# Optimization experiments

Hardware: AMD Instinct MI355X
Metric: run time of the kernel (lower is better)

## Reference

```python
import jax, jax.numpy as jnp
import numpy as np

N = 30000        # nodes
E = 480000       # edges
IN_DIM = 128
HID = 64
OUT = 64
POS_DIM = 32
H = 4            # heads (same for all layers)
PVOCAB = 3
NEG_SLOPE = 0.2


def _xavier(key, shape):
    fan_in, fan_out = shape[0], shape[-1] if len(shape) > 1 else shape[0]
    scale = 1.414 * np.sqrt(2.0 / (fan_in + fan_out))
    return jax.random.normal(key, shape, dtype=jnp.float32) * scale


def setup_inputs() -> dict:
    key = jax.random.key(0)
    ks = jax.random.split(key, 20)
    d0_in = IN_DIM + POS_DIM            # 160
    d_mid = HID * H + POS_DIM           # 288
    inp = {
        "features": jax.random.normal(ks[0], (N, IN_DIM), dtype=jnp.float32),
        # layer 0
        "W0": _xavier(ks[1], (d0_in, H * HID)),
        "al0": _xavier(ks[2], (H, HID)),
        "ar0": _xavier(ks[3], (H, HID)),
        "pe0": _xavier(ks[4], (PVOCAB, POS_DIM)),
        # layer 1
        "W1": _xavier(ks[5], (d_mid, H * HID)),
        "al1": _xavier(ks[6], (H, HID)),
        "ar1": _xavier(ks[7], (H, HID)),
        "pe1": _xavier(ks[8], (PVOCAB, POS_DIM)),
        # output layer
        "W2": _xavier(ks[9], (d_mid, H * OUT)),
        "al2": _xavier(ks[10], (H, OUT)),
        "ar2": _xavier(ks[11], (H, OUT)),
        "pe2": _xavier(ks[12], (PVOCAB, POS_DIM)),
        # graph
        "src": jax.random.randint(ks[13], (E,), 0, N, dtype=jnp.int32),
        "dst": jax.random.randint(ks[14], (E,), 0, N, dtype=jnp.int32),
        "pos": jax.random.randint(ks[15], (N,), 0, PVOCAB, dtype=jnp.int32),
    }
    return inp


def gat_layer(h, W, a_l, a_r, src, dst):
    # h: [N, in_d]; W: [in_d, H*d]; a_l,a_r: [H, d]
    n = h.shape[0]
    nh, d = a_l.shape
    ft = (h @ W).reshape(n, nh, d)                       # [N,H,d]
    a1 = jnp.einsum("nhd,hd->nh", ft, a_l)               # [N,H]
    a2 = jnp.einsum("nhd,hd->nh", ft, a_r)               # [N,H]
    e = jax.nn.leaky_relu(a1[src] + a2[dst], NEG_SLOPE)  # [E,H]
    # per-destination segment softmax (numerically stable)
    m = jax.ops.segment_max(e, dst, num_segments=n)      # [N,H]
    ex = jnp.exp(e - m[dst])                             # [E,H]
    s = jax.ops.segment_sum(ex, dst, num_segments=n)     # [N,H]
    alpha = ex / s[dst]                                  # [E,H]
    msg = ft[src] * alpha[:, :, None]                    # [E,H,d]
    return jax.ops.segment_sum(msg, dst, num_segments=n) # [N,H,d]


def reference(features, W0, al0, ar0, pe0, W1, al1, ar1, pe1,
              W2, al2, ar2, pe2, src, dst, pos):
    h = features
    # hidden GAT layers with ELU activation and head-flattening
    for W, al, ar, pe in ((W0, al0, ar0, pe0), (W1, al1, ar1, pe1)):
        p = pe[pos]                                      # [N, pos_dim]
        hcat = jnp.concatenate((h, p), axis=1)
        out = gat_layer(hcat, W, al, ar, src, dst)       # [N,H,d]
        h = jax.nn.elu(out.reshape(out.shape[0], -1))    # [N,H*d]
    # output layer: mean over heads
    p = pe2[pos]
    hcat = jnp.concatenate((h, p), axis=1)
    out = gat_layer(hcat, W2, al2, ar2, src, dst)        # [N,H,out]
    return out.mean(axis=1)                              # [N,out]
```

## Files before the change

kernel.cpp:

```cpp
#include <hip/hip_runtime.h>
#include <hip/hip_fp16.h>
#include <math.h>

#define N_NODES 30000
#define N_EDGES 480000
#define HEADS 4
#define DHEAD 64
#define FDIM 256
#define POSD 32
#define SCAN_B 1024
#define SCAN_NB ((N_NODES + SCAN_B - 1) / SCAN_B)

typedef _Float16 half8 __attribute__((ext_vector_type(8)));
typedef float floatx4 __attribute__((ext_vector_type(4)));

__device__ __forceinline__ float lrelu(float x){ return x > 0.f ? x : 0.2f * x; }

__global__ void hist_k(const int* __restrict__ dst, int* __restrict__ deg){
  int e = blockIdx.x * blockDim.x + threadIdx.x;
  if (e < N_EDGES) atomicAdd(&deg[dst[e]], 1);
}

__global__ void scanA_k(const int* __restrict__ deg, int* __restrict__ off,
                        int* __restrict__ bsum){
  __shared__ int sm[SCAN_B];
  int t = threadIdx.x;
  int i = blockIdx.x * SCAN_B + t;
  int x = (i < N_NODES) ? deg[i] : 0;
  sm[t] = x;
  __syncthreads();
#pragma unroll
  for (int o = 1; o < SCAN_B; o <<= 1){
    int v = (t >= o) ? sm[t - o] : 0;
    __syncthreads();
    sm[t] += v;
    __syncthreads();
  }
  if (i < N_NODES) off[i] = sm[t] - x;
  if (t == SCAN_B - 1) bsum[blockIdx.x] = sm[t];
}

__global__ void scanB_k(int* __restrict__ bsum, int* __restrict__ boff){
  __shared__ int sm[64];
  int t = threadIdx.x;
  int x = (t < SCAN_NB) ? bsum[t] : 0;
  sm[t] = x;
  __syncthreads();
#pragma unroll
  for (int o = 1; o < 64; o <<= 1){
    int v = (t >= o) ? sm[t - o] : 0;
    __syncthreads();
    sm[t] += v;
    __syncthreads();
  }
  if (t < SCAN_NB) boff[t] = sm[t] - x;
}

__global__ void scanC_k(int* __restrict__ off, const int* __restrict__ boff,
                        int* __restrict__ cursor){
  int i = blockIdx.x * SCAN_B + threadIdx.x;
  if (i < N_NODES){
    int v = off[i] + boff[blockIdx.x];
    off[i] = v;
    cursor[i] = v;
  }
  if (i == 0) off[N_NODES] = N_EDGES;
}

__global__ void scatter_k(const int* __restrict__ src, const int* __restrict__ dst,
                          int* __restrict__ cursor, int* __restrict__ esrc){
  int e = blockIdx.x * blockDim.x + threadIdx.x;
  if (e < N_EDGES){
    int d = dst[e];
    int p = atomicAdd(&cursor[d], 1);
    esrc[p] = src[e];
  }
}

__global__ __launch_bounds__(256) void prep_k(
    const float* __restrict__ features, _Float16* __restrict__ feat16,
    const float* __restrict__ W0, const float* __restrict__ W1,
    const float* __restrict__ W2, _Float16* __restrict__ T0,
    _Float16* __restrict__ T1, _Float16* __restrict__ T2,
    const float* __restrict__ pe0, const float* __restrict__ pe1,
    const float* __restrict__ pe2, float* __restrict__ PW){
  int blk = blockIdx.x;
  if (blk < 3750){
    int i = (blk * 256 + threadIdx.x) * 4;
    float4 v = *(const float4*)&features[i];
    struct h4s { _Float16 h[4]; } u;
    u.h[0] = (_Float16)v.x; u.h[1] = (_Float16)v.y;
    u.h[2] = (_Float16)v.z; u.h[3] = (_Float16)v.w;
    *(h4s*)&feat16[i] = u;
  } else if (blk < 3942){
    int q = blk - 3750;
    int l = q >> 6, kk0 = q & 63;
    const float* W = l == 0 ? W0 : (l == 1 ? W1 : W2);
    _Float16* T    = l == 0 ? T0 : (l == 1 ? T1 : T2);
    int K = l == 0 ? 128 : 256;
    int n = threadIdx.x;
    for (int k = kk0; k < K; k += 64)
      T[(size_t)n * K + k] = (_Float16)W[(size_t)k * FDIM + n];
  } else {
    int q = blk - 3942;
    int layer = q / 3, v = q % 3;
    const float* W  = layer == 0 ? W0 : (layer == 1 ? W1 : W2);
    const float* pe = layer == 0 ? pe0 : (layer == 1 ? pe1 : pe2);
    int K = layer == 0 ? 128 : 256;
    int j = threadIdx.x;
    float s = 0.f;
#pragma unroll
    for (int k = 0; k < POSD; k++)
      s = fmaf(pe[v * POSD + k], W[(size_t)(K + k) * FDIM + j], s);
    PW[(layer * 3 + v) * FDIM + j] = s;
  }
}

__global__ __launch_bounds__(256) void gemm_mfma_k(
    const _Float16* __restrict__ A, const _Float16* __restrict__ Wt,
    const float* __restrict__ PW, const int* __restrict__ pos,
    const float* __restrict__ al, const float* __restrict__ arw,
    _Float16* __restrict__ Ch, float* __restrict__ a1, float* __restrict__ a2,
    int K){
  int t = threadIdx.x;
  int w = t >> 6;
  int lane = t & 63;
  int lm = lane & 15;
  int kq = lane >> 4;
  int h = blockIdx.x;
  int rowBase = blockIdx.y * 256 + w * 64;
  int colBase = h * 64;

  floatx4 acc[4][4] = {};

  const _Float16* Ar[4];
#pragma unroll
  for (int r = 0; r < 4; r++)
    Ar[r] = A + (size_t)min(rowBase + r * 16 + lm, N_NODES - 1) * K;
  const _Float16* B0 = Wt + (size_t)(colBase + 0 * 16 + lm) * K;
  const _Float16* B1 = Wt + (size_t)(colBase + 1 * 16 + lm) * K;
  const _Float16* B2 = Wt + (size_t)(colBase + 2 * 16 + lm) * K;
  const _Float16* B3 = Wt + (size_t)(colBase + 3 * 16 + lm) * K;

  for (int kb = 0; kb < K; kb += 32){
    int ko = kb + kq * 8;
    half8 b0 = *(const half8*)(B0 + ko);
    half8 b1 = *(const half8*)(B1 + ko);
    half8 b2 = *(const half8*)(B2 + ko);
    half8 b3 = *(const half8*)(B3 + ko);
#pragma unroll
    for (int r = 0; r < 4; r++){
      half8 af = *(const half8*)(Ar[r] + ko);
      acc[r][0] = __builtin_amdgcn_mfma_f32_16x16x32_f16(af, b0, acc[r][0], 0, 0, 0);
      acc[r][1] = __builtin_amdgcn_mfma_f32_16x16x32_f16(af, b1, acc[r][1], 0, 0, 0);
      acc[r][2] = __builtin_amdgcn_mfma_f32_16x16x32_f16(af, b2, acc[r][2], 0, 0, 0);
      acc[r][3] = __builtin_amdgcn_mfma_f32_16x16x32_f16(af, b3, acc[r][3], 0, 0, 0);
    }
  }

  float alw[4], arr[4];
#pragma unroll
  for (int j = 0; j < 4; j++){
    alw[j] = al [h * DHEAD + j * 16 + lm];
    arr[j] = arw[h * DHEAD + j * 16 + lm];
  }

#pragma unroll
  for (int r = 0; r < 4; r++){
#pragma unroll
    for (int p = 0; p < 4; p++){
      int row = rowBase + r * 16 + kq * 4 + p;
      if (row >= N_NODES) continue;
      int pz = pos[row];
      const float* pwb = PW + pz * FDIM + colBase;
      float s1 = 0.f, s2 = 0.f;
#pragma unroll
      for (int j = 0; j < 4; j++){
        float v = acc[r][j][p] + pwb[j * 16 + lm];
        Ch[(size_t)row * FDIM + colBase + j * 16 + lm] = (_Float16)v;
        s1 = fmaf(v, alw[j], s1);
        s2 = fmaf(v, arr[j], s2);
      }
      s1 += __shfl_xor(s1, 1, 64); s2 += __shfl_xor(s2, 1, 64);
      s1 += __shfl_xor(s1, 2, 64); s2 += __shfl_xor(s2, 2, 64);
      s1 += __shfl_xor(s1, 4, 64); s2 += __shfl_xor(s2, 4, 64);
      s1 += __shfl_xor(s1, 8, 64); s2 += __shfl_xor(s2, 8, 64);
      if (lm == 0){
        a1[row * HEADS + h] = s1;
        a2[row * HEADS + h] = s2;
      }
    }
  }
}

__global__ __launch_bounds__(256) void agg4_k(
    const _Float16* __restrict__ ft, const float* __restrict__ a1,
    const float* __restrict__ a2, const int* __restrict__ off,
    const int* __restrict__ esrc, _Float16* __restrict__ outh,
    float* __restrict__ outf, int mode){
  int wv = threadIdx.x >> 6;
  int lane = threadIdx.x & 63;
  int n = blockIdx.x * 4 + wv;
  if (n >= N_NODES) return;
  int jb = off[n];
  int deg = off[n + 1] - jb;
  int eidx = lane & 15, h = lane >> 4;
  int hsel = h << 4;
  float a2n = a2[n * HEADS + h];
  float4 acc = make_float4(0.f, 0.f, 0.f, 0.f);
  const _Float16* ftl = ft + lane * 4;

  if (deg <= 64){
    int sreg[4]; float wreg[4];
    float m = -INFINITY;
#pragma unroll
    for (int r = 0; r < 4; r++){
      int idx = eidx + r * 16;
      int s = (idx < deg) ? esrc[jb + idx] : 0;
      sreg[r] = s;
      float e = (idx < deg) ? lrelu(a1[s * HEADS + h] + a2n) : -INFINITY;
      wreg[r] = e;
      m = fmaxf(m, e);
    }
    m = fmaxf(m, __shfl_xor(m, 1, 64));
    m = fmaxf(m, __shfl_xor(m, 2, 64));
    m = fmaxf(m, __shfl_xor(m, 4, 64));
    m = fmaxf(m, __shfl_xor(m, 8, 64));
    float ss = 0.f;
#pragma unroll
    for (int r = 0; r < 4; r++){
      int idx = eidx + r * 16;
      float tv = (idx < deg) ? __expf(wreg[r] - m) : 0.f;
      wreg[r] = tv;
      ss += tv;
    }
    ss += __shfl_xor(ss, 1, 64);
    ss += __shfl_xor(ss, 2, 64);
    ss += __shfl_xor(ss, 4, 64);
    ss += __shfl_xor(ss, 8, 64);
    float inv = (ss > 0.f) ? 1.f / ss : 0.f;
#pragma unroll
    for (int r = 0; r < 4; r++) wreg[r] *= inv;

#pragma unroll
    for (int r = 0; r < 4; r++){
      if (r * 16 >= deg) break;
      int lim = deg - r * 16; if (lim > 16) lim = 16;
      float wr = wreg[r]; int sr = sreg[r];
      for (int jj = 0; jj < lim; jj += 4){
#pragma unroll
        for (int u = 0; u < 4; u++){
          float wj = __shfl(wr, (jj + u) | hsel, 64);
          int sj = __shfl(sr, jj + u, 64);
          struct h4 { __half2 a, b; };
          h4 f = *(const h4*)(ftl + (size_t)sj * FDIM);
          float2 fa = __half22float2(f.a), fb = __half22float2(f.b);
          acc.x = fmaf(wj, fa.x, acc.x);
          acc.y = fmaf(wj, fa.y, acc.y);
          acc.z = fmaf(wj, fb.x, acc.z);
          acc.w = fmaf(wj, fb.y, acc.w);
        }
      }
    }
  } else {
    float m = -INFINITY;
    for (int idx = eidx; idx < deg; idx += 16){
      int s = esrc[jb + idx];
      m = fmaxf(m, lrelu(a1[s * HEADS + h] + a2n));
    }
    m = fmaxf(m, __shfl_xor(m, 1, 64));
    m = fmaxf(m, __shfl_xor(m, 2, 64));
    m = fmaxf(m, __shfl_xor(m, 4, 64));
    m = fmaxf(m, __shfl_xor(m, 8, 64));
    float ss = 0.f;
    for (int idx = eidx; idx < deg; idx += 16){
      int s = esrc[jb + idx];
      ss += __expf(lrelu(a1[s * HEADS + h] + a2n) - m);
    }
    ss += __shfl_xor(ss, 1, 64);
    ss += __shfl_xor(ss, 2, 64);
    ss += __shfl_xor(ss, 4, 64);
    ss += __shfl_xor(ss, 8, 64);
    float inv = (ss > 0.f) ? 1.f / ss : 0.f;
    for (int j = 0; j < deg; j++){
      int sj = esrc[jb + j];
      float e = lrelu(a1[sj * HEADS + h] + a2n);
      float wj = __expf(e - m) * inv;
      struct h4 { __half2 a, b; };
      h4 f = *(const h4*)(ftl + (size_t)sj * FDIM);
      float2 fa = __half22float2(f.a), fb = __half22float2(f.b);
      acc.x = fmaf(wj, fa.x, acc.x);
      acc.y = fmaf(wj, fa.y, acc.y);
      acc.z = fmaf(wj, fb.x, acc.z);
      acc.w = fmaf(wj, fb.y, acc.w);
    }
  }

  if (mode == 0){
    acc.x = acc.x > 0.f ? acc.x : (__expf(acc.x) - 1.f);
    acc.y = acc.y > 0.f ? acc.y : (__expf(acc.y) - 1.f);
    acc.z = acc.z > 0.f ? acc.z : (__expf(acc.z) - 1.f);
    acc.w = acc.w > 0.f ? acc.w : (__expf(acc.w) - 1.f);
    struct h4s { _Float16 h[4]; } u;
    u.h[0] = (_Float16)acc.x; u.h[1] = (_Float16)acc.y;
    u.h[2] = (_Float16)acc.z; u.h[3] = (_Float16)acc.w;
    *(h4s*)&outh[(size_t)n * FDIM + lane * 4] = u;
  } else {
#pragma unroll
    for (int o2 = 16; o2 <= 32; o2 <<= 1){
      acc.x += __shfl_xor(acc.x, o2, 64);
      acc.y += __shfl_xor(acc.y, o2, 64);
      acc.z += __shfl_xor(acc.z, o2, 64);
      acc.w += __shfl_xor(acc.w, o2, 64);
    }
    if (lane < 16){
      float4 o;
      o.x = acc.x * 0.25f; o.y = acc.y * 0.25f;
      o.z = acc.z * 0.25f; o.w = acc.w * 0.25f;
      *(float4*)&outf[(size_t)n * DHEAD + lane * 4] = o;
    }
  }
}

extern "C" void kernel_launch(void* const* d_in, const int* in_sizes, int n_in,
                              void* d_out, int out_size, void* d_ws, size_t ws_size,
                              hipStream_t stream){
  const float* features = (const float*)d_in[0];
  const float* W0  = (const float*)d_in[1];
  const float* al0 = (const float*)d_in[2];
  const float* ar0 = (const float*)d_in[3];
  const float* pe0 = (const float*)d_in[4];
  const float* W1  = (const float*)d_in[5];
  const float* al1 = (const float*)d_in[6];
  const float* ar1 = (const float*)d_in[7];
  const float* pe1 = (const float*)d_in[8];
  const float* W2  = (const float*)d_in[9];
  const float* al2 = (const float*)d_in[10];
  const float* ar2 = (const float*)d_in[11];
  const float* pe2 = (const float*)d_in[12];
  const int* srcv  = (const int*)d_in[13];
  const int* dstv  = (const int*)d_in[14];
  const int* posv  = (const int*)d_in[15];
  float* out = (float*)d_out;

  char* wp = (char*)d_ws;
  auto alloc = [&](size_t bytes){
    void* p = (void*)wp;
    wp += (bytes + 255) & ~(size_t)255;
    return p;
  };
  _Float16* fth   = (_Float16*)alloc(sizeof(_Float16) * (size_t)N_NODES * FDIM);
  _Float16* hbuf  = (_Float16*)alloc(sizeof(_Float16) * (size_t)N_NODES * FDIM);
  _Float16* feat16= (_Float16*)alloc(sizeof(_Float16) * (size_t)N_NODES * 128);
  _Float16* Wt0   = (_Float16*)alloc(sizeof(_Float16) * 256 * 128);
  _Float16* Wt1   = (_Float16*)alloc(sizeof(_Float16) * 256 * 256);
  _Float16* Wt2   = (_Float16*)alloc(sizeof(_Float16) * 256 * 256);
  float* a1     = (float*)alloc(sizeof(float) * N_NODES * HEADS);
  float* a2     = (float*)alloc(sizeof(float) * N_NODES * HEADS);
  float* PW     = (float*)alloc(sizeof(float) * 9 * FDIM);
  int*   deg    = (int*)alloc(sizeof(int) * N_NODES);
  int*   off    = (int*)alloc(sizeof(int) * (N_NODES + 1));
  int*   cursor = (int*)alloc(sizeof(int) * N_NODES);
  int*   bsum   = (int*)alloc(sizeof(int) * 64);
  int*   boff   = (int*)alloc(sizeof(int) * 64);
  int*   esrc   = (int*)alloc(sizeof(int) * N_EDGES);

  hipMemsetAsync(deg, 0, sizeof(int) * N_NODES, stream);
  hist_k<<<(N_EDGES + 255) / 256, 256, 0, stream>>>(dstv, deg);
  scanA_k<<<SCAN_NB, SCAN_B, 0, stream>>>(deg, off, bsum);
  scanB_k<<<1, 64, 0, stream>>>(bsum, boff);
  scanC_k<<<SCAN_NB, SCAN_B, 0, stream>>>(off, boff, cursor);
  scatter_k<<<(N_EDGES + 255) / 256, 256, 0, stream>>>(srcv, dstv, cursor, esrc);

  prep_k<<<3951, 256, 0, stream>>>(features, feat16, W0, W1, W2,
                                   Wt0, Wt1, Wt2, pe0, pe1, pe2, PW);

  dim3 ggrid(HEADS, (N_NODES + 255) / 256);
  int agrid = (N_NODES + 3) / 4;

  gemm_mfma_k<<<ggrid, 256, 0, stream>>>(feat16, Wt0, PW + 0 * 3 * FDIM, posv,
                                         al0, ar0, fth, a1, a2, 128);
  agg4_k<<<agrid, 256, 0, stream>>>(fth, a1, a2, off, esrc, hbuf, nullptr, 0);

  gemm_mfma_k<<<ggrid, 256, 0, stream>>>(hbuf, Wt1, PW + 1 * 3 * FDIM, posv,
                                         al1, ar1, fth, a1, a2, 256);
  agg4_k<<<agrid, 256, 0, stream>>>(fth, a1, a2, off, esrc, hbuf, nullptr, 0);

  gemm_mfma_k<<<ggrid, 256, 0, stream>>>(hbuf, Wt2, PW + 2 * 3 * FDIM, posv,
                                         al2, ar2, fth, a1, a2, 256);
  agg4_k<<<agrid, 256, 0, stream>>>(fth, a1, a2, off, esrc, nullptr, out, 1);
}
```

Measured before the change: 322.4 us.

## Fuse histogram into prep kernel and replace three-pass scan with single-pass scan

The degree histogram is merged into the prep kernel as extra blocks, which saves one launch and lets the atomics overlap with the feature and weight conversion. The three-kernel block scan becomes one kernel that uses wavefront shuffles. Each block gets its prefix by re-summing all earlier degrees directly, so no block-sum pass is needed. This cuts launches and global synchronisation points in CSR construction, at the cost of redundant reads of deg that grow with block index.

```diff
diff --git a/kernel.cpp b/kernel.cpp
--- a/kernel.cpp
+++ b/kernel.cpp
@@ -8,76 +8,16 @@
 #define DHEAD 64
 #define FDIM 256
 #define POSD 32
-#define SCAN_B 1024
-#define SCAN_NB ((N_NODES + SCAN_B - 1) / SCAN_B)
+#define SCAN_NB 30
+#define HIST_NB 1875
 
 typedef _Float16 half8 __attribute__((ext_vector_type(8)));
 typedef float floatx4 __attribute__((ext_vector_type(4)));
 
 __device__ __forceinline__ float lrelu(float x){ return x > 0.f ? x : 0.2f * x; }
 
-__global__ void hist_k(const int* __restrict__ dst, int* __restrict__ deg){
-  int e = blockIdx.x * blockDim.x + threadIdx.x;
-  if (e < N_EDGES) atomicAdd(&deg[dst[e]], 1);
-}
-
-__global__ void scanA_k(const int* __restrict__ deg, int* __restrict__ off,
-                        int* __restrict__ bsum){
-  __shared__ int sm[SCAN_B];
-  int t = threadIdx.x;
-  int i = blockIdx.x * SCAN_B + t;
-  int x = (i < N_NODES) ? deg[i] : 0;
-  sm[t] = x;
-  __syncthreads();
-#pragma unroll
-  for (int o = 1; o < SCAN_B; o <<= 1){
-    int v = (t >= o) ? sm[t - o] : 0;
-    __syncthreads();
-    sm[t] += v;
-    __syncthreads();
-  }
-  if (i < N_NODES) off[i] = sm[t] - x;
-  if (t == SCAN_B - 1) bsum[blockIdx.x] = sm[t];
-}
-
-__global__ void scanB_k(int* __restrict__ bsum, int* __restrict__ boff){
-  __shared__ int sm[64];
-  int t = threadIdx.x;
-  int x = (t < SCAN_NB) ? bsum[t] : 0;
-  sm[t] = x;
-  __syncthreads();
-#pragma unroll
-  for (int o = 1; o < 64; o <<= 1){
-    int v = (t >= o) ? sm[t - o] : 0;
-    __syncthreads();
-    sm[t] += v;
-    __syncthreads();
-  }
-  if (t < SCAN_NB) boff[t] = sm[t] - x;
-}
-
-__global__ void scanC_k(int* __restrict__ off, const int* __restrict__ boff,
-                        int* __restrict__ cursor){
-  int i = blockIdx.x * SCAN_B + threadIdx.x;
-  if (i < N_NODES){
-    int v = off[i] + boff[blockIdx.x];
-    off[i] = v;
-    cursor[i] = v;
-  }
-  if (i == 0) off[N_NODES] = N_EDGES;
-}
-
-__global__ void scatter_k(const int* __restrict__ src, const int* __restrict__ dst,
-                          int* __restrict__ cursor, int* __restrict__ esrc){
-  int e = blockIdx.x * blockDim.x + threadIdx.x;
-  if (e < N_EDGES){
-    int d = dst[e];
-    int p = atomicAdd(&cursor[d], 1);
-    esrc[p] = src[e];
-  }
-}
-
-__global__ __launch_bounds__(256) void prep_k(
+__global__ __launch_bounds__(256) void histprep_k(
+    const int* __restrict__ dst, int* __restrict__ deg,
     const float* __restrict__ features, _Float16* __restrict__ feat16,
     const float* __restrict__ W0, const float* __restrict__ W1,
     const float* __restrict__ W2, _Float16* __restrict__ T0,
@@ -85,15 +25,18 @@
     const float* __restrict__ pe0, const float* __restrict__ pe1,
     const float* __restrict__ pe2, float* __restrict__ PW){
   int blk = blockIdx.x;
-  if (blk < 3750){
-    int i = (blk * 256 + threadIdx.x) * 4;
+  if (blk < HIST_NB){
+    int e = blk * 256 + threadIdx.x;
+    if (e < N_EDGES) atomicAdd(&deg[dst[e]], 1);
+  } else if (blk < HIST_NB + 3750){
+    int i = ((blk - HIST_NB) * 256 + threadIdx.x) * 4;
     float4 v = *(const float4*)&features[i];
     struct h4s { _Float16 h[4]; } u;
     u.h[0] = (_Float16)v.x; u.h[1] = (_Float16)v.y;
     u.h[2] = (_Float16)v.z; u.h[3] = (_Float16)v.w;
     *(h4s*)&feat16[i] = u;
-  } else if (blk < 3942){
-    int q = blk - 3750;
+  } else if (blk < HIST_NB + 3942){
+    int q = blk - HIST_NB - 3750;
     int l = q >> 6, kk0 = q & 63;
     const float* W = l == 0 ? W0 : (l == 1 ? W1 : W2);
     _Float16* T    = l == 0 ? T0 : (l == 1 ? T1 : T2);
@@ -102,7 +45,7 @@
     for (int k = kk0; k < K; k += 64)
       T[(size_t)n * K + k] = (_Float16)W[(size_t)k * FDIM + n];
   } else {
-    int q = blk - 3942;
+    int q = blk - HIST_NB - 3942;
     int layer = q / 3, v = q % 3;
     const float* W  = layer == 0 ? W0 : (layer == 1 ? W1 : W2);
     const float* pe = layer == 0 ? pe0 : (layer == 1 ? pe1 : pe2);
@@ -113,6 +56,62 @@
     for (int k = 0; k < POSD; k++)
       s = fmaf(pe[v * POSD + k], W[(size_t)(K + k) * FDIM + j], s);
     PW[(layer * 3 + v) * FDIM + j] = s;
+  }
+}
+
+__global__ __launch_bounds__(1024) void scan_k(
+    const int* __restrict__ deg, int* __restrict__ off,
+    int* __restrict__ cursor){
+  __shared__ int wsum[16];
+  __shared__ int wpb[16];
+  int b = blockIdx.x, t = threadIdx.x;
+  int lane = t & 63, wv = t >> 6;
+  int i = b * 1024 + t;
+  int x = (i < N_NODES) ? deg[i] : 0;
+
+  int v = x;
+#pragma unroll
+  for (int o = 1; o < 64; o <<= 1){
+    int u = __shfl_up(v, o, 64);
+    if (lane >= o) v += u;
+  }
+  if (lane == 63) wsum[wv] = v;
+
+  int pb = 0;
+  for (int j = t; j < b * 1024; j += 1024) pb += deg[j];
+#pragma unroll
+  for (int o = 1; o < 64; o <<= 1) pb += __shfl_xor(pb, o, 64);
+  if (lane == 0) wpb[wv] = pb;
+  __syncthreads();
+
+  if (wv == 0){
+    int ws = (lane < 16) ? wsum[lane] : 0;
+    int sv = ws;
+#pragma unroll
+    for (int o = 1; o < 16; o <<= 1){
+      int u = __shfl_up(sv, o, 64);
+      if (lane >= o) sv += u;
+    }
+    if (lane < 16) wsum[lane] = sv - ws;
+    int bb = (lane < 16) ? wpb[lane] : 0;
+#pragma unroll
+    for (int o = 1; o < 16; o <<= 1) bb += __shfl_xor(bb, o, 64);
+    if (lane == 0) wpb[0] = bb;
+  }
+  __syncthreads();
+
+  int excl = v - x + wsum[wv] + wpb[0];
+  if (i < N_NODES){ off[i] = excl; cursor[i] = excl; }
+  if (i == 0) off[N_NODES] = N_EDGES;
+}
+
+__global__ void scatter_k(const int* __restrict__ src, const int* __restrict__ dst,
+                          int* __restrict__ cursor, int* __restrict__ esrc){
+  int e = blockIdx.x * blockDim.x + threadIdx.x;
+  if (e < N_EDGES){
+    int d = dst[e];
+    int p = atomicAdd(&cursor[d], 1);
+    esrc[p] = src[e];
   }
 }
 
@@ -361,19 +360,14 @@
   int*   deg    = (int*)alloc(sizeof(int) * N_NODES);
   int*   off    = (int*)alloc(sizeof(int) * (N_NODES + 1));
   int*   cursor = (int*)alloc(sizeof(int) * N_NODES);
-  int*   bsum   = (int*)alloc(sizeof(int) * 64);
-  int*   boff   = (int*)alloc(sizeof(int) * 64);
   int*   esrc   = (int*)alloc(sizeof(int) * N_EDGES);
 
   hipMemsetAsync(deg, 0, sizeof(int) * N_NODES, stream);
-  hist_k<<<(N_EDGES + 255) / 256, 256, 0, stream>>>(dstv, deg);
-  scanA_k<<<SCAN_NB, SCAN_B, 0, stream>>>(deg, off, bsum);
-  scanB_k<<<1, 64, 0, stream>>>(bsum, boff);
-  scanC_k<<<SCAN_NB, SCAN_B, 0, stream>>>(off, boff, cursor);
+  histprep_k<<<HIST_NB + 3951, 256, 0, stream>>>(
+      dstv, deg, features, feat16, W0, W1, W2, Wt0, Wt1, Wt2,
+      pe0, pe1, pe2, PW);
+  scan_k<<<SCAN_NB, 1024, 0, stream>>>(deg, off, cursor);
   scatter_k<<<(N_EDGES + 255) / 256, 256, 0, stream>>>(srcv, dstv, cursor, esrc);
-
-  prep_k<<<3951, 256, 0, stream>>>(features, feat16, W0, W1, W2,
-                                   Wt0, Wt1, Wt2, pe0, pe1, pe2, PW);
 
   dim3 ggrid(HEADS, (N_NODES + 255) / 256);
   int agrid = (N_NODES + 3) / 4;
```

Measured after the change: 321.0 us. About the same (-0.4%).
